# Kernel tuning notes

Measured on AMD Instinct MI355X. Metric: run time of the kernel, lower is better.

The kernel has to match this reference:

```python
import jax, jax.numpy as jnp
import numpy as np

B, N, OBS, HID, ACT = 1024, 128, 64, 128, 9


def setup_inputs() -> dict:
    key = jax.random.key(0)
    ks = jax.random.split(key, 16)
    s = 0.05
    x = jax.random.normal(ks[0], (B, N, OBS), dtype=jnp.float32)
    # binary adjacency mask with self-loops (diagonal forced to 1)
    m = (jax.random.uniform(ks[1], (B, N, N)) < 0.3).astype(jnp.float32)
    eye = jnp.eye(N, dtype=jnp.float32)
    mask = jnp.maximum(m, eye[None, :, :])
    def lin(k, din, dout):
        kw, kb = jax.random.split(k)
        return (jax.random.normal(kw, (din, dout), dtype=jnp.float32) * s,
                jax.random.normal(kb, (dout,), dtype=jnp.float32) * s)
    enc_w, enc_b = lin(ks[2], OBS, HID)
    wv, bv = lin(ks[3], HID, HID)
    wk, bk = lin(ks[4], HID, HID)
    wq, bq = lin(ks[5], HID, HID)
    w1, b1 = lin(ks[6], HID, HID)
    w2, b2 = lin(ks[7], HID, HID)
    w3, b3 = lin(ks[8], HID, HID)
    w4, b4 = lin(ks[9], HID, ACT)
    return dict(x=x, mask=mask, enc_w=enc_w, enc_b=enc_b, wv=wv, bv=bv,
                wk=wk, bk=bk, wq=wq, bq=bq, w1=w1, b1=b1, w2=w2, b2=b2,
                w3=w3, b3=b3, w4=w4, b4=b4)


def reference(x, mask, enc_w, enc_b, wv, bv, wk, bk, wq, bq,
              w1, b1, w2, b2, w3, b3, w4, b4):
    relu = jax.nn.relu
    # Encoder
    h1 = relu(x @ enc_w + enc_b)                       # [B,N,HID]
    # Masked attention (AttModel; fcout is unused in the original forward)
    v = relu(h1 @ wv + bv)
    q = relu(h1 @ wq + bq)
    k = relu(h1 @ wk + bk)
    scores = jnp.einsum('bnd,bmd->bnm', q, k)          # bmm(q, k^T)
    h = jnp.clip(scores * mask, 0.0, 9e13) - 9e15 * (1.0 - mask)
    att = jax.nn.softmax(h, axis=2)
    h2 = jnp.einsum('bnm,bmd->bnd', att, v)            # [B,N,HID]
    # Actor MLP + softmax + categorical sample
    a = relu(h2 @ w1 + b1)
    a = relu(a @ w2 + b2)
    a = relu(a @ w3 + b3)
    logits = a @ w4 + b4
    probs = jax.nn.softmax(logits, axis=-1)            # [B,N,ACT]
    actions = jax.random.categorical(jax.random.key(42), jnp.log(probs), axis=-1)
    return actions, h
```

## Files before the change

kernel.cpp:

```cpp
#include <hip/hip_runtime.h>

#define NB   1024
#define NN   128
#define NOBS 64
#define NHID 128
#define NACT 9
#define NTHR 512
#define WLD  136
#define CVS2 20

#define OFF_ENC 0
#define OFF_V   16384
#define OFF_K   49152
#define OFF_Q   81920
#define OFF_W1  114688
#define OFF_W2  147456
#define OFF_W3  180224
#define OFF_W4  212992

typedef __attribute__((ext_vector_type(8))) _Float16 half8;
typedef __attribute__((ext_vector_type(4))) _Float16 half4v;
typedef __attribute__((ext_vector_type(2))) __fp16 fp16x2;
typedef __attribute__((ext_vector_type(4))) float f32x4;

union H8 { half8 v; fp16x2 p[4]; };
union H4 { half4v v; fp16x2 p[2]; };

__global__ void prep_w(const float* __restrict__ w, _Float16* __restrict__ hi,
                       _Float16* __restrict__ lo, int din, int dout, int dpad){
  int i = blockIdx.x * blockDim.x + threadIdx.x;
  if (i >= dpad * din) return;
  int c = i / din, k = i - c * din;
  float v = (c < dout) ? w[(size_t)k * dout + c] : 0.0f;
  _Float16 h = (_Float16)v;
  hi[i] = h;
  lo[i] = (_Float16)(v - (float)h);
}

__device__ __forceinline__ void pack_split8(const float* fv, half8& ah, half8& al){
  H8 A, L;
#pragma unroll
  for (int j = 0; j < 4; ++j){
    fp16x2 h = __builtin_amdgcn_cvt_pkrtz(fv[2*j], fv[2*j+1]);
    float r0 = fv[2*j]   - (float)h[0];
    float r1 = fv[2*j+1] - (float)h[1];
    A.p[j] = h;
    L.p[j] = __builtin_amdgcn_cvt_pkrtz(r0, r1);
  }
  ah = A.v; al = L.v;
}

__device__ __forceinline__ void tf4(unsigned& v0, unsigned& v1, int r0,int r1,int r2,int r3){
  v0 += v1; v1 = (v1<<r0)|(v1>>(32-r0)); v1 ^= v0;
  v0 += v1; v1 = (v1<<r1)|(v1>>(32-r1)); v1 ^= v0;
  v0 += v1; v1 = (v1<<r2)|(v1>>(32-r2)); v1 ^= v0;
  v0 += v1; v1 = (v1<<r3)|(v1>>(32-r3)); v1 ^= v0;
}
__device__ __forceinline__ void threefry(unsigned x0, unsigned x1, unsigned& o0, unsigned& o1){
  const unsigned ks0 = 0u, ks1 = 42u, ks2 = 0x1BD11BDAu ^ 0u ^ 42u;
  unsigned v0 = x0 + ks0, v1 = x1 + ks1;
  tf4(v0,v1,13,15,26,6);  v0 += ks1; v1 += ks2 + 1u;
  tf4(v0,v1,17,29,16,24); v0 += ks2; v1 += ks0 + 2u;
  tf4(v0,v1,13,15,26,6);  v0 += ks0; v1 += ks1 + 3u;
  tf4(v0,v1,17,29,16,24); v0 += ks1; v1 += ks2 + 4u;
  tf4(v0,v1,13,15,26,6);  v0 += ks2; v1 += ks0 + 5u;
  o0 = v0; o1 = v1;
}

#define MFMA(a,b,c) __builtin_amdgcn_mfma_f32_16x16x32_f16((a),(b),(c),0,0,0)
#define MFMA3(ah,al,bh,bl,c) do{ (c)=MFMA((ah),(bh),(c)); (c)=MFMA((al),(bh),(c)); \
                                 (c)=MFMA((ah),(bl),(c)); }while(0)

__device__ __forceinline__ void zero8(f32x4* a){
#pragma unroll
  for (int c = 0; c < 8; ++c) a[c] = (f32x4){0.f,0.f,0.f,0.f};
}

template<int ROWS, int K>
__device__ __forceinline__ void stage_w(const _Float16* __restrict__ src,
                                        _Float16* dsth, _Float16* dstl, int tid){
  constexpr int GPR = K/8;
  constexpr int NG  = ROWS*GPR;
#pragma unroll
  for (int t0 = 0; t0 < NG; t0 += NTHR){
    int t = t0 + tid;
    if (NG % NTHR != 0 && t >= NG) break;
    int row = t / GPR, gc = t - row*GPR;
    int d = row*WLD + gc*8;
    *(half8*)(dsth + d) = *(const half8*)(src + t*8);
    *(half8*)(dstl + d) = *(const half8*)(src + ROWS*K + t*8);
  }
}

template<int NG>
__device__ __forceinline__ void stage_load(const _Float16* __restrict__ src, int loOff,
                                           half8* bh, half8* bl, int tid){
#pragma unroll
  for (int j = 0; j*NTHR < NG; ++j){
    int t = j*NTHR + tid;
    if (NG % NTHR != 0 && t >= NG) break;
    bh[j] = *(const half8*)(src + t*8);
    bl[j] = *(const half8*)(src + loOff + t*8);
  }
}
template<int NG, int GPR>
__device__ __forceinline__ void stage_write(const half8* bh, const half8* bl,
                                            _Float16* dsth, _Float16* dstl, int tid){
#pragma unroll
  for (int j = 0; j*NTHR < NG; ++j){
    int t = j*NTHR + tid;
    if (NG % NTHR != 0 && t >= NG) break;
    int row = t / GPR, gc = t - row*GPR;
    int d = row*WLD + gc*8;
    *(half8*)(dsth + d) = bh[j];
    *(half8*)(dstl + d) = bl[j];
  }
}

template<int K>
__device__ __forceinline__ void gemm_lds(const half8* fh, const half8* fl,
                                         const _Float16* SWh, const _Float16* SWl,
                                         f32x4* acc, int g, int l15){
  __builtin_amdgcn_s_setprio(1);
#pragma unroll
  for (int kp = 0; kp < K/32; ++kp){
#pragma unroll
    for (int c = 0; c < 8; ++c){
      const int idx = (16*c + l15)*WLD + (4*kp + g)*8;
      half8 bh = *(const half8*)(SWh + idx);
      half8 bl = *(const half8*)(SWl + idx);
      MFMA3(fh[kp], fl[kp], bh, bl, acc[c]);
    }
  }
  __builtin_amdgcn_s_setprio(0);
}

__device__ __forceinline__ void cv_row8(const f32x4* pa, int kp, float* CVf,
                                        int g, int l15, float* fv){
  const int roff = l15*CVS2 + 8*(g & 1);
#pragma unroll
  for (int i = 0; i < 4; ++i) CVf[(4*g+i)*CVS2 + l15] = pa[2*kp][i];
  f32x4 a0 = *(const f32x4*)(CVf + roff);
  f32x4 a1 = *(const f32x4*)(CVf + roff + 4);
#pragma unroll
  for (int i = 0; i < 4; ++i) CVf[(4*g+i)*CVS2 + l15] = pa[2*kp+1][i];
  f32x4 b0 = *(const f32x4*)(CVf + roff);
  f32x4 b1 = *(const f32x4*)(CVf + roff + 4);
  f32x4 f0 = (g < 2) ? a0 : b0;
  f32x4 f1 = (g < 2) ? a1 : b1;
  fv[0]=f0[0]; fv[1]=f0[1]; fv[2]=f0[2]; fv[3]=f0[3];
  fv[4]=f1[0]; fv[5]=f1[1]; fv[6]=f1[2]; fv[7]=f1[3];
}

__device__ __forceinline__ void conv_all16(const f32x4* pa, float* CVf, int g, int l15,
                                           half8* fh, half8* fl){
#pragma unroll
  for (int kp = 0; kp < 4; ++kp){
    float fv[8];
    cv_row8(pa, kp, CVf, g, l15, fv);
    pack_split8(fv, fh[kp], fl[kp]);
  }
}

__device__ __forceinline__ void gemm_cv(const f32x4* pa, float* CVf,
                                        const _Float16* SWh, const _Float16* SWl,
                                        f32x4* acc, int g, int l15){
#pragma unroll
  for (int kp = 0; kp < 4; ++kp){
    float fv[8];
    cv_row8(pa, kp, CVf, g, l15, fv);
    half8 ah, al;
    pack_split8(fv, ah, al);
    __builtin_amdgcn_s_setprio(1);
#pragma unroll
    for (int c = 0; c < 8; ++c){
      const int idx = (16*c + l15)*WLD + (4*kp + g)*8;
      half8 bh = *(const half8*)(SWh + idx);
      half8 bl = *(const half8*)(SWl + idx);
      MFMA3(ah, al, bh, bl, acc[c]);
    }
    __builtin_amdgcn_s_setprio(0);
  }
}

__device__ __forceinline__ void finalize(f32x4* acc, const float* __restrict__ bias,
                                         int l15, bool relu){
#pragma unroll
  for (int c = 0; c < 8; ++c){
    float bb = bias[16*c + l15];
#pragma unroll
    for (int i = 0; i < 4; ++i){
      float v = acc[c][i] + bb;
      acc[c][i] = relu ? fmaxf(v, 0.0f) : v;
    }
  }
}

__global__ void __launch_bounds__(NTHR)
dgn_main(const float* __restrict__ x, const float* __restrict__ mask,
         const _Float16* __restrict__ wt,
         const float* __restrict__ encb, const float* __restrict__ bv,
         const float* __restrict__ bk, const float* __restrict__ bq,
         const float* __restrict__ b1, const float* __restrict__ b2,
         const float* __restrict__ b3, const float* __restrict__ b4,
         float* __restrict__ out){
  __shared__ __align__(16) _Float16 SHh[128*WLD];
  __shared__ __align__(16) _Float16 SHl[128*WLD];
  __shared__ __align__(16) float CVA[8*16*CVS2];

  const int tid  = threadIdx.x;
  const int lane = tid & 63;
  const int w    = tid >> 6;
  const int l15  = lane & 15;
  const int g    = lane >> 4;
  const int b    = blockIdx.x;
  float* CVf = CVA + w*16*CVS2;

  f32x4 accA[8], accB[8];
  half8 wbh[4], wbl[4];

  stage_w<128, 64>(wt + OFF_ENC, SHh, SHl, tid);
  __syncthreads();

  stage_load<2048>(wt + OFF_Q, 16384, wbh, wbl, tid);
  zero8(accA);
  {
    half8 xh[2], xl[2];
    const float* xrow = x + ((size_t)b*NN + w*16 + l15)*NOBS;
#pragma unroll
    for (int kp = 0; kp < 2; ++kp){
      float4 f0 = *(const float4*)(xrow + 32*kp + 8*g);
      float4 f1 = *(const float4*)(xrow + 32*kp + 8*g + 4);
      float fv[8] = {f0.x,f0.y,f0.z,f0.w,f1.x,f1.y,f1.z,f1.w};
      pack_split8(fv, xh[kp], xl[kp]);
    }
    gemm_lds<NOBS>(xh, xl, SHh, SHl, accA, g, l15);
  }
  finalize(accA, encb, l15, true);
  half8 h1h[4], h1l[4];
  conv_all16(accA, CVf, g, l15, h1h, h1l);
  __syncthreads();
  stage_write<2048,16>(wbh, wbl, SHh, SHl, tid);
  __syncthreads();

  stage_load<2048>(wt + OFF_K, 16384, wbh, wbl, tid);
  zero8(accA);
  gemm_lds<NHID>(h1h, h1l, SHh, SHl, accA, g, l15);
  finalize(accA, bq, l15, true);
  half8 qfh[4], qfl[4];
  conv_all16(accA, CVf, g, l15, qfh, qfl);
  __syncthreads();
  stage_write<2048,16>(wbh, wbl, SHh, SHl, tid);
  __syncthreads();

  float mpre[32];
  {
    const float* mbase = mask + (size_t)b*NN*NN;
#pragma unroll
    for (int c = 0; c < 8; ++c)
#pragma unroll
      for (int i = 0; i < 4; ++i)
        mpre[c*4+i] = mbase[(w*16 + 4*g + i)*NN + 16*c + l15];
  }
  zero8(accA);
  gemm_lds<NHID>(h1h, h1l, SHh, SHl, accA, g, l15);
  finalize(accA, bk, l15, true);
  __syncthreads();
#pragma unroll
  for (int c = 0; c < 8; ++c)
#pragma unroll
    for (int i = 0; i < 4; ++i){
      float v = accA[c][i];
      _Float16 kh = (_Float16)v;
      const int idx = (w*16 + 4*g + i)*WLD + 16*c + l15;
      SHh[idx] = kh;
      SHl[idx] = (_Float16)(v - (float)kh);
    }
  __syncthreads();

  zero8(accB);
  gemm_lds<NHID>(qfh, qfl, SHh, SHl, accB, g, l15);
  __syncthreads();

  half8 afh[4], afl[4];
  {
    float* hbase = out + (size_t)NB*NN + (size_t)b*NN*NN;
    float mx[4] = {-3.0e38f,-3.0e38f,-3.0e38f,-3.0e38f};
#pragma unroll
    for (int c = 0; c < 8; ++c)
#pragma unroll
      for (int i = 0; i < 4; ++i){
        const int row = w*16 + 4*g + i, col = 16*c + l15;
        float m = mpre[c*4+i];
        float hvv = fminf(fmaxf(accB[c][i]*m, 0.0f), 9.0e13f) - 9.0e15f*(1.0f - m);
        hbase[row*NN + col] = hvv;
        accB[c][i] = hvv;
        mx[i] = fmaxf(mx[i], hvv);
      }
    stage_load<2048>(wt + OFF_V, 16384, wbh, wbl, tid);
#pragma unroll
    for (int off = 8; off >= 1; off >>= 1)
#pragma unroll
      for (int i = 0; i < 4; ++i) mx[i] = fmaxf(mx[i], __shfl_xor(mx[i], off, 64));
    float sm[4] = {0.f,0.f,0.f,0.f};
#pragma unroll
    for (int c = 0; c < 8; ++c)
#pragma unroll
      for (int i = 0; i < 4; ++i){
        float e = __expf(accB[c][i] - mx[i]);
        accB[c][i] = e; sm[i] += e;
      }
#pragma unroll
    for (int off = 8; off >= 1; off >>= 1)
#pragma unroll
      for (int i = 0; i < 4; ++i) sm[i] += __shfl_xor(sm[i], off, 64);
    float inv[4];
#pragma unroll
    for (int i = 0; i < 4; ++i) inv[i] = 16384.0f / sm[i];
#pragma unroll
    for (int c = 0; c < 8; ++c)
#pragma unroll
      for (int i = 0; i < 4; ++i) accB[c][i] *= inv[i];
    conv_all16(accB, CVf, g, l15, afh, afl);
  }
  stage_write<2048,16>(wbh, wbl, SHh, SHl, tid);
  __syncthreads();

  zero8(accA);
  gemm_lds<NHID>(h1h, h1l, SHh, SHl, accA, g, l15);
  finalize(accA, bv, l15, true);
  __syncthreads();

#pragma unroll
  for (int c = 0; c < 8; ++c){
    H4 hp, lp;
#pragma unroll
    for (int j = 0; j < 2; ++j){
      float v0 = accA[c][2*j], v1 = accA[c][2*j+1];
      fp16x2 h = __builtin_amdgcn_cvt_pkrtz(v0, v1);
      hp.p[j] = h;
      lp.p[j] = __builtin_amdgcn_cvt_pkrtz(v0 - (float)h[0], v1 - (float)h[1]);
    }
    const int idx = (16*c + l15)*WLD + w*16 + 4*g;
    *(half4v*)(SHh + idx) = hp.v;
    *(half4v*)(SHl + idx) = lp.v;
  }
  __syncthreads();

  stage_load<2048>(wt + OFF_W1, 16384, wbh, wbl, tid);
  zero8(accB);
  gemm_lds<NHID>(afh, afl, SHh, SHl, accB, g, l15);
#pragma unroll
  for (int c = 0; c < 8; ++c)
#pragma unroll
    for (int i = 0; i < 4; ++i) accB[c][i] *= 6.103515625e-05f;
  __syncthreads();
  stage_write<2048,16>(wbh, wbl, SHh, SHl, tid);
  __syncthreads();

  stage_load<2048>(wt + OFF_W2, 16384, wbh, wbl, tid);
  zero8(accA);
  gemm_cv(accB, CVf, SHh, SHl, accA, g, l15);
  finalize(accA, b1, l15, true);
  __syncthreads();
  stage_write<2048,16>(wbh, wbl, SHh, SHl, tid);
  __syncthreads();

  stage_load<2048>(wt + OFF_W3, 16384, wbh, wbl, tid);
  zero8(accB);
  gemm_cv(accA, CVf, SHh, SHl, accB, g, l15);
  finalize(accB, b2, l15, true);
  __syncthreads();
  stage_write<2048,16>(wbh, wbl, SHh, SHl, tid);
  __syncthreads();

  zero8(accA);
  gemm_cv(accB, CVf, SHh, SHl, accA, g, l15);
  finalize(accA, b3, l15, true);

  f32x4 la = (f32x4){0.f,0.f,0.f,0.f};
#pragma unroll
  for (int kp = 0; kp < 4; ++kp){
    float fv[8];
    cv_row8(accA, kp, CVf, g, l15, fv);
    half8 ah, al;
    pack_split8(fv, ah, al);
    const int wof = l15*NHID + (4*kp + g)*8;
    half8 bh = *(const half8*)(wt + OFF_W4 + wof);
    half8 bl = *(const half8*)(wt + OFF_W4 + 2048 + wof);
    MFMA3(ah, al, bh, bl, la);
  }
#pragma unroll
  for (int i = 0; i < 4; ++i)
    CVf[(4*g+i)*CVS2 + l15] = la[i] + ((l15 < NACT) ? b4[l15] : 0.0f);

  if (g == 0){
    float lg[NACT]; float mxl = -3.0e38f;
#pragma unroll
    for (int c = 0; c < NACT; ++c){ lg[c] = CVf[l15*CVS2 + c]; mxl = fmaxf(mxl, lg[c]); }
    float s = 0.f; float p[NACT];
#pragma unroll
    for (int c = 0; c < NACT; ++c){ p[c] = expf(lg[c] - mxl); s += p[c]; }
    const int R = b*NN + w*16 + l15;
    const unsigned HHALF = (unsigned)(NB*NN*NACT/2);
    float best = -3.0e38f; int bi = 0;
#pragma unroll
    for (int c = 0; c < NACT; ++c){
      float lp = logf(p[c] / s);
      unsigned e = (unsigned)(R*NACT + c);
      unsigned c0 = (e < HHALF) ? e : (e - HHALF);
      unsigned o0, o1; threefry(c0, c0 + HHALF, o0, o1);
      unsigned bits = (e < HHALF) ? o0 : o1;
      float u = __uint_as_float((bits >> 9) | 0x3f800000u) - 1.0f;
      float uu = fmaxf(1.17549435e-38f, u + 1.17549435e-38f);
      float gmb = -logf(-logf(uu));
      float scv = gmb + lp;
      if (scv > best){ best = scv; bi = c; }
    }
    out[R] = (float)bi;
  }
}

extern "C" void kernel_launch(void* const* d_in, const int* in_sizes, int n_in,
                              void* d_out, int out_size, void* d_ws, size_t ws_size,
                              hipStream_t stream){
  const float* x     = (const float*)d_in[0];
  const float* mask  = (const float*)d_in[1];
  const float* enc_w = (const float*)d_in[2];
  const float* enc_b = (const float*)d_in[3];
  const float* wv    = (const float*)d_in[4];
  const float* bv    = (const float*)d_in[5];
  const float* wk    = (const float*)d_in[6];
  const float* bk    = (const float*)d_in[7];
  const float* wq    = (const float*)d_in[8];
  const float* bq    = (const float*)d_in[9];
  const float* w1    = (const float*)d_in[10];
  const float* b1    = (const float*)d_in[11];
  const float* w2    = (const float*)d_in[12];
  const float* b2    = (const float*)d_in[13];
  const float* w3    = (const float*)d_in[14];
  const float* b3    = (const float*)d_in[15];
  const float* w4    = (const float*)d_in[16];
  const float* b4    = (const float*)d_in[17];
  _Float16* wt = (_Float16*)d_ws;
  float* out = (float*)d_out;

  prep_w<<<32, 256, 0, stream>>>(enc_w, wt+OFF_ENC, wt+OFF_ENC+8192, NOBS, NHID, NHID);
  prep_w<<<64, 256, 0, stream>>>(wv, wt+OFF_V, wt+OFF_V+16384, NHID, NHID, NHID);
  prep_w<<<64, 256, 0, stream>>>(wk, wt+OFF_K, wt+OFF_K+16384, NHID, NHID, NHID);
  prep_w<<<64, 256, 0, stream>>>(wq, wt+OFF_Q, wt+OFF_Q+16384, NHID, NHID, NHID);
  prep_w<<<64, 256, 0, stream>>>(w1, wt+OFF_W1, wt+OFF_W1+16384, NHID, NHID, NHID);
  prep_w<<<64, 256, 0, stream>>>(w2, wt+OFF_W2, wt+OFF_W2+16384, NHID, NHID, NHID);
  prep_w<<<64, 256, 0, stream>>>(w3, wt+OFF_W3, wt+OFF_W3+16384, NHID, NHID, NHID);
  prep_w<<<8,  256, 0, stream>>>(w4, wt+OFF_W4, wt+OFF_W4+2048, NHID, NACT, 16);

  dgn_main<<<NB, NTHR, 0, stream>>>(x, mask, wt, enc_b, bv, bk, bq,
                                    b1, b2, b3, b4, out);
}
```

Before: 175.1 us.

## Reorder attention stages, prefetch x early, drop redundant log-softmax before sampling

Encoder weight staging now goes through register prefetch, and the x row loads are issued early so they overlap it. Q is kept in fp32 accumulators and fed through gemm_cv instead of being converted to fp16 hi/lo registers. The V-weight and W1-weight loads are moved earlier so they overlap the QK^T and V GEMMs, and the attention probabilities are likewise consumed via gemm_cv, which frees fp16 register arrays. The log-softmax before the Gumbel argmax is dropped because subtracting a per-row constant does not change the argmax, though rounding differences could occasionally flip a near-tied sample.

```diff
diff --git a/kernel.cpp b/kernel.cpp
--- a/kernel.cpp
+++ b/kernel.cpp
@@ -74,22 +74,6 @@
 __device__ __forceinline__ void zero8(f32x4* a){
 #pragma unroll
   for (int c = 0; c < 8; ++c) a[c] = (f32x4){0.f,0.f,0.f,0.f};
-}
-
-template<int ROWS, int K>
-__device__ __forceinline__ void stage_w(const _Float16* __restrict__ src,
-                                        _Float16* dsth, _Float16* dstl, int tid){
-  constexpr int GPR = K/8;
-  constexpr int NG  = ROWS*GPR;
-#pragma unroll
-  for (int t0 = 0; t0 < NG; t0 += NTHR){
-    int t = t0 + tid;
-    if (NG % NTHR != 0 && t >= NG) break;
-    int row = t / GPR, gc = t - row*GPR;
-    int d = row*WLD + gc*8;
-    *(half8*)(dsth + d) = *(const half8*)(src + t*8);
-    *(half8*)(dstl + d) = *(const half8*)(src + ROWS*K + t*8);
-  }
 }
 
 template<int NG>
@@ -219,21 +203,24 @@
   f32x4 accA[8], accB[8];
   half8 wbh[4], wbl[4];
 
-  stage_w<128, 64>(wt + OFF_ENC, SHh, SHl, tid);
+  const float* xrow = x + ((size_t)b*NN + w*16 + l15)*NOBS;
+  float4 xf[4];
+  xf[0] = *(const float4*)(xrow + 8*g);
+  xf[1] = *(const float4*)(xrow + 8*g + 4);
+  xf[2] = *(const float4*)(xrow + 32 + 8*g);
+  xf[3] = *(const float4*)(xrow + 32 + 8*g + 4);
+  stage_load<1024>(wt + OFF_ENC, 8192, wbh, wbl, tid);
+  stage_write<1024,8>(wbh, wbl, SHh, SHl, tid);
   __syncthreads();
 
   stage_load<2048>(wt + OFF_Q, 16384, wbh, wbl, tid);
   zero8(accA);
   {
     half8 xh[2], xl[2];
-    const float* xrow = x + ((size_t)b*NN + w*16 + l15)*NOBS;
-#pragma unroll
-    for (int kp = 0; kp < 2; ++kp){
-      float4 f0 = *(const float4*)(xrow + 32*kp + 8*g);
-      float4 f1 = *(const float4*)(xrow + 32*kp + 8*g + 4);
-      float fv[8] = {f0.x,f0.y,f0.z,f0.w,f1.x,f1.y,f1.z,f1.w};
-      pack_split8(fv, xh[kp], xl[kp]);
-    }
+    float fv0[8] = {xf[0].x,xf[0].y,xf[0].z,xf[0].w,xf[1].x,xf[1].y,xf[1].z,xf[1].w};
+    float fv1[8] = {xf[2].x,xf[2].y,xf[2].z,xf[2].w,xf[3].x,xf[3].y,xf[3].z,xf[3].w};
+    pack_split8(fv0, xh[0], xl[0]);
+    pack_split8(fv1, xh[1], xl[1]);
     gemm_lds<NOBS>(xh, xl, SHh, SHl, accA, g, l15);
   }
   finalize(accA, encb, l15, true);
@@ -244,11 +231,9 @@
   __syncthreads();
 
   stage_load<2048>(wt + OFF_K, 16384, wbh, wbl, tid);
-  zero8(accA);
-  gemm_lds<NHID>(h1h, h1l, SHh, SHl, accA, g, l15);
-  finalize(accA, bq, l15, true);
-  half8 qfh[4], qfl[4];
-  conv_all16(accA, CVf, g, l15, qfh, qfl);
+  zero8(accB);
+  gemm_lds<NHID>(h1h, h1l, SHh, SHl, accB, g, l15);
+  finalize(accB, bq, l15, true);
   __syncthreads();
   stage_write<2048,16>(wbh, wbl, SHh, SHl, tid);
   __syncthreads();
@@ -278,11 +263,12 @@
     }
   __syncthreads();
 
-  zero8(accB);
-  gemm_lds<NHID>(qfh, qfl, SHh, SHl, accB, g, l15);
-  __syncthreads();
-
-  half8 afh[4], afl[4];
+  stage_load<2048>(wt + OFF_V, 16384, wbh, wbl, tid);
+  zero8(accA);
+  gemm_cv(accB, CVf, SHh, SHl, accA, g, l15);
+  __syncthreads();
+
+  stage_write<2048,16>(wbh, wbl, SHh, SHl, tid);
   {
     float* hbase = out + (size_t)NB*NN + (size_t)b*NN*NN;
     float mx[4] = {-3.0e38f,-3.0e38f,-3.0e38f,-3.0e38f};
@@ -292,12 +278,11 @@
       for (int i = 0; i < 4; ++i){
         const int row = w*16 + 4*g + i, col = 16*c + l15;
         float m = mpre[c*4+i];
-        float hvv = fminf(fmaxf(accB[c][i]*m, 0.0f), 9.0e13f) - 9.0e15f*(1.0f - m);
+        float hvv = fminf(fmaxf(accA[c][i]*m, 0.0f), 9.0e13f) - 9.0e15f*(1.0f - m);
         hbase[row*NN + col] = hvv;
-        accB[c][i] = hvv;
+        accA[c][i] = hvv;
         mx[i] = fmaxf(mx[i], hvv);
       }
-    stage_load<2048>(wt + OFF_V, 16384, wbh, wbl, tid);
 #pragma unroll
     for (int off = 8; off >= 1; off >>= 1)
 #pragma unroll
@@ -307,8 +292,8 @@
     for (int c = 0; c < 8; ++c)
 #pragma unroll
       for (int i = 0; i < 4; ++i){
-        float e = __expf(accB[c][i] - mx[i]);
-        accB[c][i] = e; sm[i] += e;
+        float e = __expf(accA[c][i] - mx[i]);
+        accA[c][i] = e; sm[i] += e;
       }
 #pragma unroll
     for (int off = 8; off >= 1; off >>= 1)
@@ -320,15 +305,14 @@
 #pragma unroll
     for (int c = 0; c < 8; ++c)
 #pragma unroll
-      for (int i = 0; i < 4; ++i) accB[c][i] *= inv[i];
-    conv_all16(accB, CVf, g, l15, afh, afl);
-  }
-  stage_write<2048,16>(wbh, wbl, SHh, SHl, tid);
-  __syncthreads();
-
-  zero8(accA);
-  gemm_lds<NHID>(h1h, h1l, SHh, SHl, accA, g, l15);
-  finalize(accA, bv, l15, true);
+      for (int i = 0; i < 4; ++i) accA[c][i] *= inv[i];
+  }
+  __syncthreads();
+
+  stage_load<2048>(wt + OFF_W1, 16384, wbh, wbl, tid);
+  zero8(accB);
+  gemm_lds<NHID>(h1h, h1l, SHh, SHl, accB, g, l15);
+  finalize(accB, bv, l15, true);
   __syncthreads();
 
 #pragma unroll
@@ -336,7 +320,7 @@
     H4 hp, lp;
 #pragma unroll
     for (int j = 0; j < 2; ++j){
-      float v0 = accA[c][2*j], v1 = accA[c][2*j+1];
+      float v0 = accB[c][2*j], v1 = accB[c][2*j+1];
       fp16x2 h = __builtin_amdgcn_cvt_pkrtz(v0, v1);
       hp.p[j] = h;
       lp.p[j] = __builtin_amdgcn_cvt_pkrtz(v0 - (float)h[0], v1 - (float)h[1]);
@@ -347,9 +331,8 @@
   }
   __syncthreads();
 
-  stage_load<2048>(wt + OFF_W1, 16384, wbh, wbl, tid);
   zero8(accB);
-  gemm_lds<NHID>(afh, afl, SHh, SHl, accB, g, l15);
+  gemm_cv(accA, CVf, SHh, SHl, accB, g, l15);
 #pragma unroll
   for (int c = 0; c < 8; ++c)
 #pragma unroll
@@ -395,18 +378,12 @@
     CVf[(4*g+i)*CVS2 + l15] = la[i] + ((l15 < NACT) ? b4[l15] : 0.0f);
 
   if (g == 0){
-    float lg[NACT]; float mxl = -3.0e38f;
-#pragma unroll
-    for (int c = 0; c < NACT; ++c){ lg[c] = CVf[l15*CVS2 + c]; mxl = fmaxf(mxl, lg[c]); }
-    float s = 0.f; float p[NACT];
-#pragma unroll
-    for (int c = 0; c < NACT; ++c){ p[c] = expf(lg[c] - mxl); s += p[c]; }
     const int R = b*NN + w*16 + l15;
     const unsigned HHALF = (unsigned)(NB*NN*NACT/2);
     float best = -3.0e38f; int bi = 0;
 #pragma unroll
     for (int c = 0; c < NACT; ++c){
-      float lp = logf(p[c] / s);
+      float lg = CVf[l15*CVS2 + c];
       unsigned e = (unsigned)(R*NACT + c);
       unsigned c0 = (e < HHALF) ? e : (e - HHALF);
       unsigned o0, o1; threefry(c0, c0 + HHALF, o0, o1);
@@ -414,7 +391,7 @@
       float u = __uint_as_float((bits >> 9) | 0x3f800000u) - 1.0f;
       float uu = fmaxf(1.17549435e-38f, u + 1.17549435e-38f);
       float gmb = -logf(-logf(uu));
-      float scv = gmb + lp;
+      float scv = gmb + lg;
       if (scv > best){ best = scv; bi = c; }
     }
     out[R] = (float)bi;
```

Result: no change. 177.2 us (+1.2%).

## Fold biases into accumulator init and spread Gumbel sampling across all lanes

Applied to the files above, without the earlier changes.

Biases are now loaded early and used to initialise the MFMA accumulators, so the post-GEMM finalize pass only applies ReLU. The categorical sampling tail drops the softmax/log normalisation, since argmax of Gumbel plus logits is shift invariant. Its nine threefry+log evaluations are split across the four lane groups, then combined with a cross-group shuffle argmax. This removes serial work from a quarter of the lanes but adds shuffles and a tie-break rule that must match the original first-max choice.

```diff
diff --git a/kernel.cpp b/kernel.cpp
--- a/kernel.cpp
+++ b/kernel.cpp
@@ -75,6 +75,20 @@
 #pragma unroll
   for (int c = 0; c < 8; ++c) a[c] = (f32x4){0.f,0.f,0.f,0.f};
 }
+__device__ __forceinline__ void load_bias8(const float* __restrict__ bias, int l15, float* bb){
+#pragma unroll
+  for (int c = 0; c < 8; ++c) bb[c] = bias[16*c + l15];
+}
+__device__ __forceinline__ void init8(f32x4* a, const float* bb){
+#pragma unroll
+  for (int c = 0; c < 8; ++c) a[c] = (f32x4){bb[c], bb[c], bb[c], bb[c]};
+}
+__device__ __forceinline__ void relu8(f32x4* a){
+#pragma unroll
+  for (int c = 0; c < 8; ++c)
+#pragma unroll
+    for (int i = 0; i < 4; ++i) a[c][i] = fmaxf(a[c][i], 0.0f);
+}
 
 template<int ROWS, int K>
 __device__ __forceinline__ void stage_w(const _Float16* __restrict__ src,
@@ -180,19 +194,6 @@
       MFMA3(ah, al, bh, bl, acc[c]);
     }
     __builtin_amdgcn_s_setprio(0);
-  }
-}
-
-__device__ __forceinline__ void finalize(f32x4* acc, const float* __restrict__ bias,
-                                         int l15, bool relu){
-#pragma unroll
-  for (int c = 0; c < 8; ++c){
-    float bb = bias[16*c + l15];
-#pragma unroll
-    for (int i = 0; i < 4; ++i){
-      float v = acc[c][i] + bb;
-      acc[c][i] = relu ? fmaxf(v, 0.0f) : v;
-    }
   }
 }
 
@@ -218,12 +219,15 @@
 
   f32x4 accA[8], accB[8];
   half8 wbh[4], wbl[4];
-
+  float bb[8];
+
+  load_bias8(encb, l15, bb);
   stage_w<128, 64>(wt + OFF_ENC, SHh, SHl, tid);
   __syncthreads();
 
+  init8(accA, bb);
   stage_load<2048>(wt + OFF_Q, 16384, wbh, wbl, tid);
-  zero8(accA);
+  load_bias8(bq, l15, bb);
   {
     half8 xh[2], xl[2];
     const float* xrow = x + ((size_t)b*NN + w*16 + l15)*NOBS;
@@ -236,17 +240,18 @@
     }
     gemm_lds<NOBS>(xh, xl, SHh, SHl, accA, g, l15);
   }
-  finalize(accA, encb, l15, true);
+  relu8(accA);
   half8 h1h[4], h1l[4];
   conv_all16(accA, CVf, g, l15, h1h, h1l);
   __syncthreads();
   stage_write<2048,16>(wbh, wbl, SHh, SHl, tid);
   __syncthreads();
 
+  init8(accA, bb);
   stage_load<2048>(wt + OFF_K, 16384, wbh, wbl, tid);
-  zero8(accA);
+  load_bias8(bk, l15, bb);
   gemm_lds<NHID>(h1h, h1l, SHh, SHl, accA, g, l15);
-  finalize(accA, bq, l15, true);
+  relu8(accA);
   half8 qfh[4], qfl[4];
   conv_all16(accA, CVf, g, l15, qfh, qfl);
   __syncthreads();
@@ -262,9 +267,9 @@
       for (int i = 0; i < 4; ++i)
         mpre[c*4+i] = mbase[(w*16 + 4*g + i)*NN + 16*c + l15];
   }
-  zero8(accA);
+  init8(accA, bb);
   gemm_lds<NHID>(h1h, h1l, SHh, SHl, accA, g, l15);
-  finalize(accA, bk, l15, true);
+  relu8(accA);
   __syncthreads();
 #pragma unroll
   for (int c = 0; c < 8; ++c)
@@ -298,6 +303,7 @@
         mx[i] = fmaxf(mx[i], hvv);
       }
     stage_load<2048>(wt + OFF_V, 16384, wbh, wbl, tid);
+    load_bias8(bv, l15, bb);
 #pragma unroll
     for (int off = 8; off >= 1; off >>= 1)
 #pragma unroll
@@ -326,9 +332,9 @@
   stage_write<2048,16>(wbh, wbl, SHh, SHl, tid);
   __syncthreads();
 
-  zero8(accA);
+  init8(accA, bb);
   gemm_lds<NHID>(h1h, h1l, SHh, SHl, accA, g, l15);
-  finalize(accA, bv, l15, true);
+  relu8(accA);
   __syncthreads();
 
 #pragma unroll
@@ -348,6 +354,7 @@
   __syncthreads();
 
   stage_load<2048>(wt + OFF_W1, 16384, wbh, wbl, tid);
+  load_bias8(b1, l15, bb);
   zero8(accB);
   gemm_lds<NHID>(afh, afl, SHh, SHl, accB, g, l15);
 #pragma unroll
@@ -358,27 +365,30 @@
   stage_write<2048,16>(wbh, wbl, SHh, SHl, tid);
   __syncthreads();
 
+  init8(accA, bb);
   stage_load<2048>(wt + OFF_W2, 16384, wbh, wbl, tid);
-  zero8(accA);
+  load_bias8(b2, l15, bb);
   gemm_cv(accB, CVf, SHh, SHl, accA, g, l15);
-  finalize(accA, b1, l15, true);
-  __syncthreads();
-  stage_write<2048,16>(wbh, wbl, SHh, SHl, tid);
-  __syncthreads();
-
+  relu8(accA);
+  __syncthreads();
+  stage_write<2048,16>(wbh, wbl, SHh, SHl, tid);
+  __syncthreads();
+
+  init8(accB, bb);
   stage_load<2048>(wt + OFF_W3, 16384, wbh, wbl, tid);
-  zero8(accB);
+  load_bias8(b3, l15, bb);
+  float b4v = (l15 < NACT) ? b4[l15] : 0.0f;
   gemm_cv(accA, CVf, SHh, SHl, accB, g, l15);
-  finalize(accB, b2, l15, true);
-  __syncthreads();
-  stage_write<2048,16>(wbh, wbl, SHh, SHl, tid);
-  __syncthreads();
-
-  zero8(accA);
+  relu8(accB);
+  __syncthreads();
+  stage_write<2048,16>(wbh, wbl, SHh, SHl, tid);
+  __syncthreads();
+
+  init8(accA, bb);
   gemm_cv(accB, CVf, SHh, SHl, accA, g, l15);
-  finalize(accA, b3, l15, true);
-
-  f32x4 la = (f32x4){0.f,0.f,0.f,0.f};
+  relu8(accA);
+
+  f32x4 la = (f32x4){b4v, b4v, b4v, b4v};
 #pragma unroll
   for (int kp = 0; kp < 4; ++kp){
     float fv[8];
@@ -392,32 +402,35 @@
   }
 #pragma unroll
   for (int i = 0; i < 4; ++i)
-    CVf[(4*g+i)*CVS2 + l15] = la[i] + ((l15 < NACT) ? b4[l15] : 0.0f);
-
-  if (g == 0){
-    float lg[NACT]; float mxl = -3.0e38f;
-#pragma unroll
-    for (int c = 0; c < NACT; ++c){ lg[c] = CVf[l15*CVS2 + c]; mxl = fmaxf(mxl, lg[c]); }
-    float s = 0.f; float p[NACT];
-#pragma unroll
-    for (int c = 0; c < NACT; ++c){ p[c] = expf(lg[c] - mxl); s += p[c]; }
+    CVf[(4*g+i)*CVS2 + l15] = la[i];
+
+  {
     const int R = b*NN + w*16 + l15;
     const unsigned HHALF = (unsigned)(NB*NN*NACT/2);
-    float best = -3.0e38f; int bi = 0;
-#pragma unroll
-    for (int c = 0; c < NACT; ++c){
-      float lp = logf(p[c] / s);
-      unsigned e = (unsigned)(R*NACT + c);
-      unsigned c0 = (e < HHALF) ? e : (e - HHALF);
-      unsigned o0, o1; threefry(c0, c0 + HHALF, o0, o1);
-      unsigned bits = (e < HHALF) ? o0 : o1;
-      float u = __uint_as_float((bits >> 9) | 0x3f800000u) - 1.0f;
-      float uu = fmaxf(1.17549435e-38f, u + 1.17549435e-38f);
-      float gmb = -logf(-logf(uu));
-      float scv = gmb + lp;
-      if (scv > best){ best = scv; bi = c; }
-    }
-    out[R] = (float)bi;
+    float best = -3.0e38f; int bi = NACT;
+#pragma unroll
+    for (int j = 0; j < 3; ++j){
+      const int c = g + 4*j;
+      if (c < NACT){
+        float lg = CVf[l15*CVS2 + c];
+        unsigned e = (unsigned)(R*NACT + c);
+        unsigned c0 = (e < HHALF) ? e : (e - HHALF);
+        unsigned o0, o1; threefry(c0, c0 + HHALF, o0, o1);
+        unsigned bits = (e < HHALF) ? o0 : o1;
+        float u = __uint_as_float((bits >> 9) | 0x3f800000u) - 1.0f;
+        float uu = fmaxf(1.17549435e-38f, u + 1.17549435e-38f);
+        float gmb = -logf(-logf(uu));
+        float scv = gmb + lg;
+        if (scv > best){ best = scv; bi = c; }
+      }
+    }
+#pragma unroll
+    for (int off = 16; off <= 32; off <<= 1){
+      float ov = __shfl_xor(best, off, 64);
+      int   oi = __shfl_xor(bi,   off, 64);
+      if (ov > best || (ov == best && oi < bi)){ best = ov; bi = oi; }
+    }
+    if (g == 0) out[R] = (float)bi;
   }
 }
 
```

Result: faster. 164.9 us, median of 3 (-5.8%).
